# Kernel tuning notes

Measured on AMD Instinct MI355X. Metric: run time of the kernel, lower is better.

The kernel has to match this reference:

```python
import jax, jax.numpy as jnp
import numpy as np

N, E = 100000, 1600000
IN_C, HID, OUT_C = 128, 16, 32
H1, H2 = 8, 8  # heads for conv1/conv2; conv3 has 1 head, concat=False
NEG_SLOPE = 0.2


def setup_inputs() -> dict:
    key = jax.random.key(0)
    ks = jax.random.split(key, 16)
    def p(k, shape, fan_in):
        return jax.random.normal(k, shape, jnp.float32) * (1.0 / np.sqrt(fan_in))
    inp = {
        "x": jax.random.normal(ks[0], (N, IN_C), jnp.float32),
        "edge_index": jax.random.randint(ks[1], (2, E), 0, N, jnp.int32),
        # conv1: in=128 -> heads=8, ch=16, concat
        "W1": p(ks[2], (IN_C, H1 * HID), IN_C),
        "a_src1": p(ks[3], (H1, HID), HID),
        "a_dst1": p(ks[4], (H1, HID), HID),
        "b1": jnp.zeros((H1 * HID,), jnp.float32),
        # conv2: in=128 -> heads=8, ch=16, concat
        "W2": p(ks[5], (H1 * HID, H2 * HID), H1 * HID),
        "a_src2": p(ks[6], (H2, HID), HID),
        "a_dst2": p(ks[7], (H2, HID), HID),
        "b2": jnp.zeros((H2 * HID,), jnp.float32),
        # conv3: in=128 -> heads=1, ch=32, concat=False
        "W3": p(ks[8], (H2 * HID, OUT_C), H2 * HID),
        "a_src3": p(ks[9], (1, OUT_C), OUT_C),
        "a_dst3": p(ks[10], (1, OUT_C), OUT_C),
        "b3": jnp.zeros((OUT_C,), jnp.float32),
    }
    return inp


def gat_conv(x, src, dst, W, a_src, a_dst, b, heads, ch, concat):
    """PyG-style GATConv (eval mode): gather -> leaky_relu -> segment softmax -> scatter sum."""
    n = x.shape[0]
    h = (x @ W).reshape(n, heads, ch)                 # [N, H, C]
    al_s = jnp.sum(h * a_src, axis=-1)                # [N, H] source-side logit part
    al_d = jnp.sum(h * a_dst, axis=-1)                # [N, H] dest-side logit part
    logits = jax.nn.leaky_relu(al_s[src] + al_d[dst], NEG_SLOPE)  # [Etot, H]
    m = jax.ops.segment_max(logits, dst, num_segments=n)         # per-dest max (self loops guarantee >=1 edge)
    e = jnp.exp(logits - m[dst])
    denom = jax.ops.segment_sum(e, dst, num_segments=n)
    alpha = e / denom[dst]                            # [Etot, H]
    msgs = h[src] * alpha[..., None]                  # [Etot, H, C]
    out = jax.ops.segment_sum(msgs, dst, num_segments=n)  # [N, H, C]
    if concat:
        return out.reshape(n, heads * ch) + b
    return out.mean(axis=1) + b


def reference(x, edge_index, W1, a_src1, a_dst1, b1, W2, a_src2, a_dst2, b2,
              W3, a_src3, a_dst3, b3):
    n = x.shape[0]
    loops = jnp.arange(n, dtype=edge_index.dtype)     # PyG add_self_loops=True
    src = jnp.concatenate([edge_index[0], loops])
    dst = jnp.concatenate([edge_index[1], loops])
    h = jax.nn.relu(gat_conv(x, src, dst, W1, a_src1, a_dst1, b1, H1, HID, True))
    h = jax.nn.relu(gat_conv(h, src, dst, W2, a_src2, a_dst2, b2, H2, HID, True))
    h = gat_conv(h, src, dst, W3, a_src3, a_dst3, b3, 1, OUT_C, False)
    # global_mean_pool with all-zero batch vector -> mean over all nodes
    return h.mean(axis=0, keepdims=True)              # [1, OUT_C]
```

## Files before the change

kernel.cpp:

```cpp
#include <hip/hip_runtime.h>


typedef unsigned short bfu;
typedef unsigned char u8;
typedef __attribute__((ext_vector_type(8))) short bf16x8;
typedef __attribute__((ext_vector_type(4))) float f32x4;
typedef __attribute__((ext_vector_type(2))) float f32x2;
typedef __attribute__((ext_vector_type(4))) int i32x4;

constexpr int N_NODES = 100000;
constexpr int E_IN    = 1600000;
constexpr int E_TOT   = E_IN + N_NODES;
constexpr float NEG   = 0.2f;
constexpr int P_XCD   = 8;
constexpr int PSZ     = N_NODES / P_XCD;
constexpr int CAP     = 64;
constexpr int AGG32_B = N_NODES / 32;
constexpr int AGG128_B = N_NODES / 32;
constexpr int GEMM_B  = (N_NODES + 63) / 64;
constexpr int EDGE_B4 = (E_TOT / 4 + 255) / 256;
constexpr int FILL_B  = EDGE_B4 * P_XCD;
constexpr int PREP_ITEMS = 43008;
constexpr int PREP_B  = (PREP_ITEMS + 255) / 256;

__device__ inline bfu f2bf(float f) {
    union { float f; unsigned i; } c; c.f = f;
    unsigned x = c.i;
    return (bfu)((x + 0x7fffu + ((x >> 16) & 1u)) >> 16);
}
__device__ inline u8 f2fp8(float f) {
    return (u8)(__builtin_amdgcn_cvt_pk_fp8_f32(f, f, 0, false) & 0xff);
}


__device__ inline void prep_body(int idx,
        const float* __restrict__ W1, const float* __restrict__ W2,
        const float* __restrict__ W3,
        const float* __restrict__ as1, const float* __restrict__ ad1,
        const float* __restrict__ as2, const float* __restrict__ ad2,
        const float* __restrict__ as3, const float* __restrict__ ad3,
        bfu* __restrict__ WtX1, bfu* __restrict__ WtX2, bfu* __restrict__ WtX3) {
    if (idx < 16384) {
        int k = idx >> 7, n = idx & 127;
        WtX1[n * 128 + k] = f2bf(W1[idx]);
    } else if (idx < 32768) {
        int r = idx - 16384;
        int k = r >> 7, n = r & 127;
        WtX2[n * 128 + k] = f2bf(W2[r]);
    } else if (idx < 36864) {
        int r = idx - 32768;
        int k = r >> 5, n = r & 31;
        WtX3[n * 128 + k] = f2bf(W3[r]);
    } else if (idx < 38912) {
        int r = idx - 36864;
        int sd = r >> 10, rr = r & 1023;
        int h = rr >> 7, k = rr & 127;
        const float* a = sd ? ad1 : as1;
        float v = 0.f;
        #pragma unroll
        for (int c = 0; c < 16; ++c) v += W1[k * 128 + h * 16 + c] * a[h * 16 + c];
        WtX1[(128 + sd * 8 + h) * 128 + k] = f2bf(v);
    } else if (idx < 40960) {
        int r = idx - 38912;
        int sd = r >> 10, rr = r & 1023;
        int h = rr >> 7, k = rr & 127;
        const float* a = sd ? ad2 : as2;
        float v = 0.f;
        #pragma unroll
        for (int c = 0; c < 16; ++c) v += W2[k * 128 + h * 16 + c] * a[h * 16 + c];
        WtX2[(128 + sd * 8 + h) * 128 + k] = f2bf(v);
    } else if (idx < 41216) {
        int r = idx - 40960;
        int sd = r >> 7, k = r & 127;
        const float* a = sd ? ad3 : as3;
        float v = 0.f;
        #pragma unroll
        for (int c = 0; c < 32; ++c) v += W3[k * 32 + c] * a[c];
        WtX3[(32 + sd) * 128 + k] = f2bf(v);
    } else if (idx < 43008) {
        WtX3[34 * 128 + (idx - 41216)] = 0;
    }
}

__global__ __launch_bounds__(256) void prep_cursor(
        const float* __restrict__ W1, const float* __restrict__ W2,
        const float* __restrict__ W3,
        const float* __restrict__ as1, const float* __restrict__ ad1,
        const float* __restrict__ as2, const float* __restrict__ ad2,
        const float* __restrict__ as3, const float* __restrict__ ad3,
        bfu* __restrict__ WtX1, bfu* __restrict__ WtX2, bfu* __restrict__ WtX3,
        int* __restrict__ cursor, float* __restrict__ outp) {
    int idx = blockIdx.x * 256 + threadIdx.x;
    prep_body(idx, W1, W2, W3, as1, ad1, as2, ad2, as3, ad3, WtX1, WtX2, WtX3);
    for (int i = idx; i < N_NODES; i += PREP_ITEMS) cursor[i] = 0;
    if (idx < 32) outp[idx] = 0.f;
}


__global__ __launch_bounds__(256) void fill(const int* __restrict__ ei,
        int* __restrict__ cursor, int* __restrict__ srclist) {
    int p = blockIdx.x & 7;
    int b = blockIdx.x >> 3;
    int lo = p * PSZ, hi = lo + PSZ;
    int e0 = (b * 256 + threadIdx.x) * 4;
    if (e0 >= E_TOT) return;
    bool self = e0 >= E_IN;
    i32x4 d4, s4;
    if (!self) {
        d4 = __builtin_nontemporal_load((const i32x4*)&ei[E_IN + e0]);
        s4 = __builtin_nontemporal_load((const i32x4*)&ei[e0]);
    } else {
        int bb = e0 - E_IN;
        d4[0] = bb; d4[1] = bb + 1; d4[2] = bb + 2; d4[3] = bb + 3;
        s4 = d4;
    }
    int pos[4];
    #pragma unroll
    for (int q = 0; q < 4; ++q) {
        int d = d4[q];
        pos[q] = (d >= lo && d < hi) ? atomicAdd(&cursor[d], 1) : -1;
    }
    #pragma unroll
    for (int q = 0; q < 4; ++q) {
        if (pos[q] >= 0 && pos[q] < CAP)
            srclist[d4[q] * CAP + pos[q]] = s4[q];
    }
}


__device__ inline bf16x8 ldcvt_f32(const float* p) {
    float4 v0 = *(const float4*)p;
    float4 v1 = *(const float4*)(p + 4);
    bf16x8 a;
    a[0] = (short)f2bf(v0.x); a[1] = (short)f2bf(v0.y);
    a[2] = (short)f2bf(v0.z); a[3] = (short)f2bf(v0.w);
    a[4] = (short)f2bf(v1.x); a[5] = (short)f2bf(v1.y);
    a[6] = (short)f2bf(v1.z); a[7] = (short)f2bf(v1.w);
    return a;
}

template<int NTO, bool F32A>
__global__ __launch_bounds__(256) void gemm_mfma(const void* __restrict__ Xg_,
                                                 const bfu* __restrict__ Wt,
                                                 u8* __restrict__ Y,
                                                 float* __restrict__ als,
                                                 float* __restrict__ ald) {
    constexpr int COUT = NTO * 16;
    int wid  = threadIdx.x >> 6;
    int lane = threadIdx.x & 63;
    int m = lane & 15, quad = lane >> 4;
    int rbase = (blockIdx.x * 4 + wid) * 16;
    if (rbase >= N_NODES) return;
    int rA = rbase + m; if (rA >= N_NODES) rA = N_NODES - 1;

    bf16x8 a0, a1, a2, a3;
    if constexpr (F32A) {
        const float* Ap = (const float*)Xg_ + (size_t)rA * 128 + quad * 8;
        a0 = ldcvt_f32(Ap);
        a1 = ldcvt_f32(Ap + 32);
        a2 = ldcvt_f32(Ap + 64);
        a3 = ldcvt_f32(Ap + 96);
    } else {
        const bfu* Ap = (const bfu*)Xg_ + (size_t)rA * 128 + quad * 8;
        a0 = *(const bf16x8*)(Ap);
        a1 = *(const bf16x8*)(Ap + 32);
        a2 = *(const bf16x8*)(Ap + 64);
        a3 = *(const bf16x8*)(Ap + 96);
    }

    const bfu* Bp = Wt + (size_t)m * 128 + quad * 8;
    f32x4 acc[NTO + 1];
    #pragma unroll
    for (int nt = 0; nt <= NTO; nt++) {
        const bfu* Bn = Bp + nt * 16 * 128;
        f32x4 c = {0.f, 0.f, 0.f, 0.f};
        c = __builtin_amdgcn_mfma_f32_16x16x32_bf16(a0, *(const bf16x8*)(Bn),      c, 0, 0, 0);
        c = __builtin_amdgcn_mfma_f32_16x16x32_bf16(a1, *(const bf16x8*)(Bn + 32), c, 0, 0, 0);
        c = __builtin_amdgcn_mfma_f32_16x16x32_bf16(a2, *(const bf16x8*)(Bn + 64), c, 0, 0, 0);
        c = __builtin_amdgcn_mfma_f32_16x16x32_bf16(a3, *(const bf16x8*)(Bn + 96), c, 0, 0, 0);
        acc[nt] = c;
    }

    #pragma unroll
    for (int nt = 0; nt < NTO; nt++) {
        #pragma unroll
        for (int r = 0; r < 4; r++) {
            int row = rbase + quad * 4 + r;
            if (row < N_NODES)
                Y[(size_t)row * COUT + nt * 16 + m] = f2fp8(acc[nt][r]);
        }
    }
    #pragma unroll
    for (int r = 0; r < 4; r++) {
        int row = rbase + quad * 4 + r;
        if (row >= N_NODES) continue;
        float v = acc[NTO][r];
        if constexpr (NTO == 8) {
            if (m < 8) als[row * 8 + m] = v;
            else       ald[row * 8 + (m - 8)] = v;
        } else {
            if (m == 0) als[row] = v;
            else if (m == 1) ald[row] = v;
        }
    }
}


__device__ inline void unpack_fma(uint4 u, float w, float* a) {
    f32x2 p;
    p = __builtin_amdgcn_cvt_pk_f32_fp8((int)u.x, false); a[0]=fmaf(w,p[0],a[0]);  a[1]=fmaf(w,p[1],a[1]);
    p = __builtin_amdgcn_cvt_pk_f32_fp8((int)u.x, true);  a[2]=fmaf(w,p[0],a[2]);  a[3]=fmaf(w,p[1],a[3]);
    p = __builtin_amdgcn_cvt_pk_f32_fp8((int)u.y, false); a[4]=fmaf(w,p[0],a[4]);  a[5]=fmaf(w,p[1],a[5]);
    p = __builtin_amdgcn_cvt_pk_f32_fp8((int)u.y, true);  a[6]=fmaf(w,p[0],a[6]);  a[7]=fmaf(w,p[1],a[7]);
    p = __builtin_amdgcn_cvt_pk_f32_fp8((int)u.z, false); a[8]=fmaf(w,p[0],a[8]);  a[9]=fmaf(w,p[1],a[9]);
    p = __builtin_amdgcn_cvt_pk_f32_fp8((int)u.z, true);  a[10]=fmaf(w,p[0],a[10]); a[11]=fmaf(w,p[1],a[11]);
    p = __builtin_amdgcn_cvt_pk_f32_fp8((int)u.w, false); a[12]=fmaf(w,p[0],a[12]); a[13]=fmaf(w,p[1],a[13]);
    p = __builtin_amdgcn_cvt_pk_f32_fp8((int)u.w, true);  a[14]=fmaf(w,p[0],a[14]); a[15]=fmaf(w,p[1],a[15]);
}

__global__ __launch_bounds__(256) void agg128(const u8* __restrict__ Hb,
        const float* __restrict__ als, const float* __restrict__ ald,
        const int* __restrict__ deg, const int* __restrict__ srclist,
        const float* __restrict__ bias, bfu* __restrict__ out) {
    int wave = blockIdx.x * 4 + (threadIdx.x >> 6);
    int lane = threadIdx.x & 63;
    int sub  = lane >> 3;
    int li   = lane & 7;
    int d    = wave * 8 + sub;
    int c0   = li * 16;
    float ad = ald[d * 8 + li];
    const int* sl = srclist + d * CAP;
    int n = deg[d]; n = n < CAP ? n : CAP;
    float a[16];
    #pragma unroll
    for (int k = 0; k < 16; ++k) a[k] = 0.f;
    float den = 0.f;
    int j = 0;
    for (; j + 2 <= n; j += 2) {
        int s0 = sl[j], s1 = sl[j + 1];
        uint4 u0 = *(const uint4*)(Hb + (size_t)s0 * 128 + c0);
        uint4 u1 = *(const uint4*)(Hb + (size_t)s1 * 128 + c0);
        float x0 = als[s0 * 8 + li], x1 = als[s1 * 8 + li];
        float l0 = x0 + ad; l0 = fmaxf(l0, NEG * l0); float w0 = __expf(l0);
        float l1 = x1 + ad; l1 = fmaxf(l1, NEG * l1); float w1 = __expf(l1);
        den += w0 + w1;
        unpack_fma(u0, w0, a);
        unpack_fma(u1, w1, a);
    }
    if (j < n) {
        int s0 = sl[j];
        uint4 u0 = *(const uint4*)(Hb + (size_t)s0 * 128 + c0);
        float x0 = als[s0 * 8 + li];
        float l0 = x0 + ad; l0 = fmaxf(l0, NEG * l0); float w0 = __expf(l0);
        den += w0;
        unpack_fma(u0, w0, a);
    }
    float r = 1.f / den;
    unsigned dw[8];
    #pragma unroll
    for (int k = 0; k < 8; ++k) {
        float e0 = fmaxf(fmaf(a[2*k],   r, bias[c0 + 2*k]),   0.f);
        float e1 = fmaxf(fmaf(a[2*k+1], r, bias[c0 + 2*k+1]), 0.f);
        dw[k] = (unsigned)f2bf(e0) | ((unsigned)f2bf(e1) << 16);
    }
    uint4 st0 = {dw[0], dw[1], dw[2], dw[3]};
    uint4 st1 = {dw[4], dw[5], dw[6], dw[7]};
    *(uint4*)&out[(size_t)d * 128 + c0]     = st0;
    *(uint4*)&out[(size_t)d * 128 + c0 + 8] = st1;
}

__global__ __launch_bounds__(256) void agg32(const u8* __restrict__ Hb,
        const float* __restrict__ als, const float* __restrict__ ald,
        const int* __restrict__ deg, const int* __restrict__ srclist,
        const float* __restrict__ bias, float* __restrict__ outp) {
    __shared__ float lds[4][32];
    int t    = threadIdx.x;
    int wid  = t >> 6;
    int lane = t & 63;
    int sub  = lane >> 3;
    int li   = lane & 7;
    int d    = blockIdx.x * 32 + wid * 8 + sub;
    int c0 = li * 4;
    float adv = ald[d];
    const int* sl = srclist + d * CAP;
    int n = deg[d]; n = n < CAP ? n : CAP;
    float a0=0.f,a1=0.f,a2=0.f,a3=0.f,den=0.f;
    int j = 0;
    for (; j + 4 <= n; j += 4) {
        int s0 = sl[j], s1 = sl[j+1], s2 = sl[j+2], s3 = sl[j+3];
        unsigned u0 = *(const unsigned*)(Hb + (size_t)s0 * 32 + c0);
        unsigned u1 = *(const unsigned*)(Hb + (size_t)s1 * 32 + c0);
        unsigned u2 = *(const unsigned*)(Hb + (size_t)s2 * 32 + c0);
        unsigned u3 = *(const unsigned*)(Hb + (size_t)s3 * 32 + c0);
        float x0 = als[s0], x1 = als[s1], x2 = als[s2], x3 = als[s3];
        float l0 = x0 + adv; l0 = fmaxf(l0, NEG*l0); float w0 = __expf(l0);
        float l1 = x1 + adv; l1 = fmaxf(l1, NEG*l1); float w1 = __expf(l1);
        float l2 = x2 + adv; l2 = fmaxf(l2, NEG*l2); float w2 = __expf(l2);
        float l3 = x3 + adv; l3 = fmaxf(l3, NEG*l3); float w3 = __expf(l3);
        den += (w0 + w1) + (w2 + w3);
        f32x2 p;
        p = __builtin_amdgcn_cvt_pk_f32_fp8((int)u0, false); a0=fmaf(w0,p[0],a0); a1=fmaf(w0,p[1],a1);
        p = __builtin_amdgcn_cvt_pk_f32_fp8((int)u0, true);  a2=fmaf(w0,p[0],a2); a3=fmaf(w0,p[1],a3);
        p = __builtin_amdgcn_cvt_pk_f32_fp8((int)u1, false); a0=fmaf(w1,p[0],a0); a1=fmaf(w1,p[1],a1);
        p = __builtin_amdgcn_cvt_pk_f32_fp8((int)u1, true);  a2=fmaf(w1,p[0],a2); a3=fmaf(w1,p[1],a3);
        p = __builtin_amdgcn_cvt_pk_f32_fp8((int)u2, false); a0=fmaf(w2,p[0],a0); a1=fmaf(w2,p[1],a1);
        p = __builtin_amdgcn_cvt_pk_f32_fp8((int)u2, true);  a2=fmaf(w2,p[0],a2); a3=fmaf(w2,p[1],a3);
        p = __builtin_amdgcn_cvt_pk_f32_fp8((int)u3, false); a0=fmaf(w3,p[0],a0); a1=fmaf(w3,p[1],a1);
        p = __builtin_amdgcn_cvt_pk_f32_fp8((int)u3, true);  a2=fmaf(w3,p[0],a2); a3=fmaf(w3,p[1],a3);
    }
    for (; j < n; ++j) {
        int s0 = sl[j];
        unsigned u0 = *(const unsigned*)(Hb + (size_t)s0 * 32 + c0);
        float x0 = als[s0];
        float l0 = x0 + adv; l0 = fmaxf(l0, NEG*l0); float w0 = __expf(l0);
        den += w0;
        f32x2 p;
        p = __builtin_amdgcn_cvt_pk_f32_fp8((int)u0, false); a0=fmaf(w0,p[0],a0); a1=fmaf(w0,p[1],a1);
        p = __builtin_amdgcn_cvt_pk_f32_fp8((int)u0, true);  a2=fmaf(w0,p[0],a2); a3=fmaf(w0,p[1],a3);
    }
    float r = 1.f / den;
    float4 bv = *(const float4*)&bias[c0];
    float o0 = fmaf(a0, r, bv.x), o1 = fmaf(a1, r, bv.y);
    float o2 = fmaf(a2, r, bv.z), o3 = fmaf(a3, r, bv.w);
    #pragma unroll
    for (int mask = 8; mask < 64; mask <<= 1) {
        o0 += __shfl_xor(o0, mask);
        o1 += __shfl_xor(o1, mask);
        o2 += __shfl_xor(o2, mask);
        o3 += __shfl_xor(o3, mask);
    }
    if (sub == 0) {
        lds[wid][c0]     = o0;
        lds[wid][c0 + 1] = o1;
        lds[wid][c0 + 2] = o2;
        lds[wid][c0 + 3] = o3;
    }
    __syncthreads();
    if (t < 32)
        atomicAdd(&outp[t],
            (lds[0][t] + lds[1][t] + lds[2][t] + lds[3][t]) * (1.0f / N_NODES));
}


extern "C" void kernel_launch(void* const* d_in, const int* in_sizes, int n_in,
                              void* d_out, int out_size, void* d_ws, size_t ws_size,
                              hipStream_t stream) {
    (void)in_sizes; (void)n_in; (void)out_size; (void)ws_size;
    const float* x   = (const float*)d_in[0];
    const int*   ei  = (const int*)d_in[1];
    const float* W1  = (const float*)d_in[2];
    const float* as1 = (const float*)d_in[3];
    const float* ad1 = (const float*)d_in[4];
    const float* b1  = (const float*)d_in[5];
    const float* W2  = (const float*)d_in[6];
    const float* as2 = (const float*)d_in[7];
    const float* ad2 = (const float*)d_in[8];
    const float* b2  = (const float*)d_in[9];
    const float* W3  = (const float*)d_in[10];
    const float* as3 = (const float*)d_in[11];
    const float* ad3 = (const float*)d_in[12];
    const float* b3  = (const float*)d_in[13];

    char* ws = (char*)d_ws;
    size_t off = 0;
    auto carve = [&](size_t bytes) { void* p = ws + off; off += (bytes + 255) & ~size_t(255); return p; };
    u8*    bufH    = (u8*)carve(size_t(N_NODES) * 128);
    bfu*   bufF    = (bfu*)carve(size_t(N_NODES) * 128 * 2);
    float* als     = (float*)carve(size_t(N_NODES) * 8 * 4);
    float* ald     = (float*)carve(size_t(N_NODES) * 8 * 4);
    int*   cursor  = (int*)carve(size_t(N_NODES) * 4);
    bfu*   WtX1    = (bfu*)carve(144 * 128 * 2);
    bfu*   WtX2    = (bfu*)carve(144 * 128 * 2);
    bfu*   WtX3    = (bfu*)carve(48 * 128 * 2);
    int*   srclist = (int*)carve(size_t(N_NODES) * CAP * 4);

    prep_cursor<<<PREP_B, 256, 0, stream>>>(W1, W2, W3,
        as1, ad1, as2, ad2, as3, ad3, WtX1, WtX2, WtX3, cursor, (float*)d_out);

    fill<<<FILL_B, 256, 0, stream>>>(ei, cursor, srclist);

    gemm_mfma<8, true><<<GEMM_B, 256, 0, stream>>>(x, WtX1, bufH, als, ald);
    agg128<<<AGG128_B, 256, 0, stream>>>(bufH, als, ald, cursor, srclist, b1, bufF);

    gemm_mfma<8, false><<<GEMM_B, 256, 0, stream>>>(bufF, WtX2, bufH, als, ald);
    agg128<<<AGG128_B, 256, 0, stream>>>(bufH, als, ald, cursor, srclist, b2, bufF);

    gemm_mfma<2, false><<<GEMM_B, 256, 0, stream>>>(bufF, WtX3, bufH, als, ald);
    agg32<<<AGG32_B, 256, 0, stream>>>(bufH, als, ald, cursor, srclist, b3, (float*)d_out);
}
```

Before: 438.4 us.

## Fuse GAT aggregation with next layer's GEMM via LDS-staged tile

Merges each 128-wide aggregation kernel with the following layer's MFMA projection. Each block aggregates 64 destination nodes, writes the bf16 rows into a swizzled LDS tile, and feeds that tile straight into the GEMM. The goal is to drop the bf16 intermediate round-trip through global memory and two kernel launches. Ping-pong H/alpha buffers are added so a kernel never reads the buffers it writes. Per-block aggregation work is now 16 nodes per wave, with a barrier before the GEMM, which may hurt latency hiding.

```diff
diff --git a/kernel.cpp b/kernel.cpp
--- a/kernel.cpp
+++ b/kernel.cpp
@@ -16,8 +16,8 @@
 constexpr int PSZ     = N_NODES / P_XCD;
 constexpr int CAP     = 64;
 constexpr int AGG32_B = N_NODES / 32;
-constexpr int AGG128_B = N_NODES / 32;
 constexpr int GEMM_B  = (N_NODES + 63) / 64;
+constexpr int FUSE_B  = (N_NODES + 63) / 64;
 constexpr int EDGE_B4 = (E_TOT / 4 + 255) / 256;
 constexpr int FILL_B  = EDGE_B4 * P_XCD;
 constexpr int PREP_ITEMS = 43008;
@@ -139,13 +139,13 @@
     return a;
 }
 
-template<int NTO, bool F32A>
-__global__ __launch_bounds__(256) void gemm_mfma(const void* __restrict__ Xg_,
-                                                 const bfu* __restrict__ Wt,
-                                                 u8* __restrict__ Y,
-                                                 float* __restrict__ als,
-                                                 float* __restrict__ ald) {
-    constexpr int COUT = NTO * 16;
+__global__ __launch_bounds__(256) void gemm_mfma_l1(const float* __restrict__ Xg,
+                                                    const bfu* __restrict__ Wt,
+                                                    u8* __restrict__ Y,
+                                                    float* __restrict__ als,
+                                                    float* __restrict__ ald) {
+    constexpr int NTO = 8;
+    constexpr int COUT = 128;
     int wid  = threadIdx.x >> 6;
     int lane = threadIdx.x & 63;
     int m = lane & 15, quad = lane >> 4;
@@ -153,20 +153,11 @@
     if (rbase >= N_NODES) return;
     int rA = rbase + m; if (rA >= N_NODES) rA = N_NODES - 1;
 
-    bf16x8 a0, a1, a2, a3;
-    if constexpr (F32A) {
-        const float* Ap = (const float*)Xg_ + (size_t)rA * 128 + quad * 8;
-        a0 = ldcvt_f32(Ap);
-        a1 = ldcvt_f32(Ap + 32);
-        a2 = ldcvt_f32(Ap + 64);
-        a3 = ldcvt_f32(Ap + 96);
-    } else {
-        const bfu* Ap = (const bfu*)Xg_ + (size_t)rA * 128 + quad * 8;
-        a0 = *(const bf16x8*)(Ap);
-        a1 = *(const bf16x8*)(Ap + 32);
-        a2 = *(const bf16x8*)(Ap + 64);
-        a3 = *(const bf16x8*)(Ap + 96);
-    }
+    const float* Ap = Xg + (size_t)rA * 128 + quad * 8;
+    bf16x8 a0 = ldcvt_f32(Ap);
+    bf16x8 a1 = ldcvt_f32(Ap + 32);
+    bf16x8 a2 = ldcvt_f32(Ap + 64);
+    bf16x8 a3 = ldcvt_f32(Ap + 96);
 
     const bfu* Bp = Wt + (size_t)m * 128 + quad * 8;
     f32x4 acc[NTO + 1];
@@ -195,13 +186,8 @@
         int row = rbase + quad * 4 + r;
         if (row >= N_NODES) continue;
         float v = acc[NTO][r];
-        if constexpr (NTO == 8) {
-            if (m < 8) als[row * 8 + m] = v;
-            else       ald[row * 8 + (m - 8)] = v;
-        } else {
-            if (m == 0) als[row] = v;
-            else if (m == 1) ald[row] = v;
-        }
+        if (m < 8) als[row * 8 + m] = v;
+        else       ald[row * 8 + (m - 8)] = v;
     }
 }
 
@@ -218,56 +204,120 @@
     p = __builtin_amdgcn_cvt_pk_f32_fp8((int)u.w, true);  a[14]=fmaf(w,p[0],a[14]); a[15]=fmaf(w,p[1],a[15]);
 }
 
-__global__ __launch_bounds__(256) void agg128(const u8* __restrict__ Hb,
-        const float* __restrict__ als, const float* __restrict__ ald,
+template<int NTO>
+__global__ __launch_bounds__(256) void fused_agg_gemm(
+        const u8* __restrict__ Hin,
+        const float* __restrict__ als_in,
+        const float* __restrict__ ald_in,
         const int* __restrict__ deg, const int* __restrict__ srclist,
-        const float* __restrict__ bias, bfu* __restrict__ out) {
-    int wave = blockIdx.x * 4 + (threadIdx.x >> 6);
-    int lane = threadIdx.x & 63;
+        const float* __restrict__ bias,
+        const bfu* __restrict__ Wt,
+        u8* __restrict__ Yout,
+        float* __restrict__ als_out, float* __restrict__ ald_out) {
+    __shared__ uint4 ldsb[64 * 16];
+    int t    = threadIdx.x;
+    int wid  = t >> 6;
+    int lane = t & 63;
     int sub  = lane >> 3;
     int li   = lane & 7;
-    int d    = wave * 8 + sub;
-    int c0   = li * 16;
-    float ad = ald[d * 8 + li];
-    const int* sl = srclist + d * CAP;
-    int n = deg[d]; n = n < CAP ? n : CAP;
-    float a[16];
-    #pragma unroll
-    for (int k = 0; k < 16; ++k) a[k] = 0.f;
-    float den = 0.f;
-    int j = 0;
-    for (; j + 2 <= n; j += 2) {
-        int s0 = sl[j], s1 = sl[j + 1];
-        uint4 u0 = *(const uint4*)(Hb + (size_t)s0 * 128 + c0);
-        uint4 u1 = *(const uint4*)(Hb + (size_t)s1 * 128 + c0);
-        float x0 = als[s0 * 8 + li], x1 = als[s1 * 8 + li];
-        float l0 = x0 + ad; l0 = fmaxf(l0, NEG * l0); float w0 = __expf(l0);
-        float l1 = x1 + ad; l1 = fmaxf(l1, NEG * l1); float w1 = __expf(l1);
-        den += w0 + w1;
-        unpack_fma(u0, w0, a);
-        unpack_fma(u1, w1, a);
-    }
-    if (j < n) {
-        int s0 = sl[j];
-        uint4 u0 = *(const uint4*)(Hb + (size_t)s0 * 128 + c0);
-        float x0 = als[s0 * 8 + li];
-        float l0 = x0 + ad; l0 = fmaxf(l0, NEG * l0); float w0 = __expf(l0);
-        den += w0;
-        unpack_fma(u0, w0, a);
-    }
-    float r = 1.f / den;
-    unsigned dw[8];
-    #pragma unroll
-    for (int k = 0; k < 8; ++k) {
-        float e0 = fmaxf(fmaf(a[2*k],   r, bias[c0 + 2*k]),   0.f);
-        float e1 = fmaxf(fmaf(a[2*k+1], r, bias[c0 + 2*k+1]), 0.f);
-        dw[k] = (unsigned)f2bf(e0) | ((unsigned)f2bf(e1) << 16);
-    }
-    uint4 st0 = {dw[0], dw[1], dw[2], dw[3]};
-    uint4 st1 = {dw[4], dw[5], dw[6], dw[7]};
-    *(uint4*)&out[(size_t)d * 128 + c0]     = st0;
-    *(uint4*)&out[(size_t)d * 128 + c0 + 8] = st1;
-}
+    int rbase = blockIdx.x * 64;
+
+    #pragma unroll
+    for (int it = 0; it < 2; ++it) {
+        int dl = wid * 16 + it * 8 + sub;
+        int d  = rbase + dl;
+        if (d < N_NODES) {
+            int c0 = li * 16;
+            float ad = ald_in[d * 8 + li];
+            const int* sl = srclist + d * CAP;
+            int n = deg[d]; n = n < CAP ? n : CAP;
+            float a[16];
+            #pragma unroll
+            for (int k = 0; k < 16; ++k) a[k] = 0.f;
+            float den = 0.f;
+            int j = 0;
+            for (; j + 2 <= n; j += 2) {
+                int s0 = sl[j], s1 = sl[j + 1];
+                uint4 u0 = *(const uint4*)(Hin + (size_t)s0 * 128 + c0);
+                uint4 u1 = *(const uint4*)(Hin + (size_t)s1 * 128 + c0);
+                float x0 = als_in[s0 * 8 + li], x1 = als_in[s1 * 8 + li];
+                float l0 = x0 + ad; l0 = fmaxf(l0, NEG * l0); float w0 = __expf(l0);
+                float l1 = x1 + ad; l1 = fmaxf(l1, NEG * l1); float w1 = __expf(l1);
+                den += w0 + w1;
+                unpack_fma(u0, w0, a);
+                unpack_fma(u1, w1, a);
+            }
+            if (j < n) {
+                int s0 = sl[j];
+                uint4 u0 = *(const uint4*)(Hin + (size_t)s0 * 128 + c0);
+                float x0 = als_in[s0 * 8 + li];
+                float l0 = x0 + ad; l0 = fmaxf(l0, NEG * l0); float w0 = __expf(l0);
+                den += w0;
+                unpack_fma(u0, w0, a);
+            }
+            float r = 1.f / den;
+            unsigned dw[8];
+            #pragma unroll
+            for (int k = 0; k < 8; ++k) {
+                float e0 = fmaxf(fmaf(a[2*k],   r, bias[c0 + 2*k]),   0.f);
+                float e1 = fmaxf(fmaf(a[2*k+1], r, bias[c0 + 2*k+1]), 0.f);
+                dw[k] = (unsigned)f2bf(e0) | ((unsigned)f2bf(e1) << 16);
+            }
+            uint4 st0 = {dw[0], dw[1], dw[2], dw[3]};
+            uint4 st1 = {dw[4], dw[5], dw[6], dw[7]};
+            int sw = dl & 7;
+            ldsb[dl * 16 + ((li * 2)     ^ sw)] = st0;
+            ldsb[dl * 16 + ((li * 2 + 1) ^ sw)] = st1;
+        }
+    }
+    __syncthreads();
+
+    constexpr int COUT = NTO * 16;
+    int m = lane & 15, quad = lane >> 4;
+    int lr = wid * 16 + m;
+    int lb = lr * 16, sw = lr & 7;
+    bf16x8 a0 = *(const bf16x8*)&ldsb[lb + ((quad)      ^ sw)];
+    bf16x8 a1 = *(const bf16x8*)&ldsb[lb + ((quad + 4)  ^ sw)];
+    bf16x8 a2 = *(const bf16x8*)&ldsb[lb + ((quad + 8)  ^ sw)];
+    bf16x8 a3 = *(const bf16x8*)&ldsb[lb + ((quad + 12) ^ sw)];
+
+    const bfu* Bp = Wt + (size_t)m * 128 + quad * 8;
+    f32x4 acc[NTO + 1];
+    #pragma unroll
+    for (int nt = 0; nt <= NTO; nt++) {
+        const bfu* Bn = Bp + nt * 16 * 128;
+        f32x4 c = {0.f, 0.f, 0.f, 0.f};
+        c = __builtin_amdgcn_mfma_f32_16x16x32_bf16(a0, *(const bf16x8*)(Bn),      c, 0, 0, 0);
+        c = __builtin_amdgcn_mfma_f32_16x16x32_bf16(a1, *(const bf16x8*)(Bn + 32), c, 0, 0, 0);
+        c = __builtin_amdgcn_mfma_f32_16x16x32_bf16(a2, *(const bf16x8*)(Bn + 64), c, 0, 0, 0);
+        c = __builtin_amdgcn_mfma_f32_16x16x32_bf16(a3, *(const bf16x8*)(Bn + 96), c, 0, 0, 0);
+        acc[nt] = c;
+    }
+
+    #pragma unroll
+    for (int nt = 0; nt < NTO; nt++) {
+        #pragma unroll
+        for (int r = 0; r < 4; r++) {
+            int row = rbase + wid * 16 + quad * 4 + r;
+            if (row < N_NODES)
+                Yout[(size_t)row * COUT + nt * 16 + m] = f2fp8(acc[nt][r]);
+        }
+    }
+    #pragma unroll
+    for (int r = 0; r < 4; r++) {
+        int row = rbase + wid * 16 + quad * 4 + r;
+        if (row >= N_NODES) continue;
+        float v = acc[NTO][r];
+        if constexpr (NTO == 8) {
+            if (m < 8) als_out[row * 8 + m] = v;
+            else       ald_out[row * 8 + (m - 8)] = v;
+        } else {
+            if (m == 0) als_out[row] = v;
+            else if (m == 1) ald_out[row] = v;
+        }
+    }
+}
+
 
 __global__ __launch_bounds__(256) void agg32(const u8* __restrict__ Hb,
         const float* __restrict__ als, const float* __restrict__ ald,
@@ -364,10 +414,12 @@
     char* ws = (char*)d_ws;
     size_t off = 0;
     auto carve = [&](size_t bytes) { void* p = ws + off; off += (bytes + 255) & ~size_t(255); return p; };
-    u8*    bufH    = (u8*)carve(size_t(N_NODES) * 128);
-    bfu*   bufF    = (bfu*)carve(size_t(N_NODES) * 128 * 2);
-    float* als     = (float*)carve(size_t(N_NODES) * 8 * 4);
-    float* ald     = (float*)carve(size_t(N_NODES) * 8 * 4);
+    u8*    bufHa   = (u8*)carve(size_t(N_NODES) * 128);
+    u8*    bufHb   = (u8*)carve(size_t(N_NODES) * 128);
+    float* alsA    = (float*)carve(size_t(N_NODES) * 8 * 4);
+    float* aldA    = (float*)carve(size_t(N_NODES) * 8 * 4);
+    float* alsB    = (float*)carve(size_t(N_NODES) * 8 * 4);
+    float* aldB    = (float*)carve(size_t(N_NODES) * 8 * 4);
     int*   cursor  = (int*)carve(size_t(N_NODES) * 4);
     bfu*   WtX1    = (bfu*)carve(144 * 128 * 2);
     bfu*   WtX2    = (bfu*)carve(144 * 128 * 2);
@@ -379,12 +431,13 @@
 
     fill<<<FILL_B, 256, 0, stream>>>(ei, cursor, srclist);
 
-    gemm_mfma<8, true><<<GEMM_B, 256, 0, stream>>>(x, WtX1, bufH, als, ald);
-    agg128<<<AGG128_B, 256, 0, stream>>>(bufH, als, ald, cursor, srclist, b1, bufF);
-
-    gemm_mfma<8, false><<<GEMM_B, 256, 0, stream>>>(bufF, WtX2, bufH, als, ald);
-    agg128<<<AGG128_B, 256, 0, stream>>>(bufH, als, ald, cursor, srclist, b2, bufF);
-
-    gemm_mfma<2, false><<<GEMM_B, 256, 0, stream>>>(bufF, WtX3, bufH, als, ald);
-    agg32<<<AGG32_B, 256, 0, stream>>>(bufH, als, ald, cursor, srclist, b3, (float*)d_out);
-}
+    gemm_mfma_l1<<<GEMM_B, 256, 0, stream>>>(x, WtX1, bufHa, alsA, aldA);
+
+    fused_agg_gemm<8><<<FUSE_B, 256, 0, stream>>>(bufHa, alsA, aldA,
+        cursor, srclist, b1, WtX2, bufHb, alsB, aldB);
+
+    fused_agg_gemm<2><<<FUSE_B, 256, 0, stream>>>(bufHb, alsB, aldB,
+        cursor, srclist, b2, WtX3, bufHa, alsA, aldA);
+
+    agg32<<<AGG32_B, 256, 0, stream>>>(bufHa, alsA, aldA, cursor, srclist, b3, (float*)d_out);
+}
```

Result: no change. 430.2 us (-1.9%).
